# Kernel tuning notes

Measured on AMD Instinct MI355X. Metric: run time of the kernel, lower is better.

The kernel has to match this reference:

```python
import jax, jax.numpy as jnp
import numpy as np

B, S, H = 4, 16, 4096          # batch, new query tokens, hidden
NH, NKV, HD = 32, 8, 128       # query heads, kv heads, head_dim
PAST = 8192                    # cached kv length
ROPE_BASE = 10000.0


def setup_inputs() -> dict:
    key = jax.random.key(0)
    ks = jax.random.split(key, 7)
    wscale = 0.02
    hidden_states = jax.random.normal(ks[0], (B, S, H), jnp.float32)
    k_cache = jax.random.normal(ks[1], (B, PAST, NKV, HD), jnp.float32)
    v_cache = jax.random.normal(ks[2], (B, PAST, NKV, HD), jnp.float32)
    Wq = jax.random.normal(ks[3], (H, NH * HD), jnp.float32) * wscale
    Wk = jax.random.normal(ks[4], (H, NKV * HD), jnp.float32) * wscale
    Wv = jax.random.normal(ks[5], (H, NKV * HD), jnp.float32) * wscale
    Wo = jax.random.normal(ks[6], (NH * HD, H), jnp.float32) * wscale
    position_ids = PAST + jnp.tile(jnp.arange(S, dtype=jnp.int32)[None, :], (B, 1))
    return {"hidden_states": hidden_states, "k_cache": k_cache, "v_cache": v_cache,
            "Wq": Wq, "Wk": Wk, "Wv": Wv, "Wo": Wo, "position_ids": position_ids}


def _rotate_half(x):
    h = x.shape[-1] // 2
    return jnp.concatenate([-x[..., h:], x[..., :h]], axis=-1)


def reference(hidden_states, k_cache, v_cache, Wq, Wk, Wv, Wo, position_ids):
    b, s, _ = hidden_states.shape
    # projections -> [b, heads, s, hd]
    q = (hidden_states @ Wq).reshape(b, s, NH, HD).transpose(0, 2, 1, 3)
    k = (hidden_states @ Wk).reshape(b, s, NKV, HD).transpose(0, 2, 1, 3)
    v = (hidden_states @ Wv).reshape(b, s, NKV, HD).transpose(0, 2, 1, 3)
    # RoPE (LlamaRotaryEmbedding: base=10000, half-split rotate)
    inv_freq = 1.0 / (ROPE_BASE ** (jnp.arange(0, HD, 2, dtype=jnp.float32) / HD))
    ang = position_ids.astype(jnp.float32)[..., None] * inv_freq      # [b, s, hd/2]
    emb = jnp.concatenate([ang, ang], axis=-1)                        # [b, s, hd]
    cos = jnp.cos(emb)[:, None]                                       # [b, 1, s, hd]
    sin = jnp.sin(emb)[:, None]
    q = q * cos + _rotate_half(q) * sin
    k = k * cos + _rotate_half(k) * sin
    # kv-cache concat: cache stored [b, past, nkv, hd] -> [b, nkv, K, hd]
    k_all = jnp.concatenate([k_cache.transpose(0, 2, 1, 3), k], axis=2)
    v_all = jnp.concatenate([v_cache.transpose(0, 2, 1, 3), v], axis=2)
    # GQA repeat_kv (repeat_interleave along head dim)
    n_rep = NH // NKV
    k_all = jnp.repeat(k_all, n_rep, axis=1)                          # [b, NH, K, hd]
    v_all = jnp.repeat(v_all, n_rep, axis=1)
    K = k_all.shape[2]
    scale = HD ** -0.5
    scores = jnp.einsum('bhqd,bhkd->bhqk', q, k_all) * scale          # [b, NH, s, K]
    # flash varlen causal with seqlen_q < seqlen_k: bottom-right aligned mask
    allow = jnp.arange(K)[None, :] <= (K - s + jnp.arange(s))[:, None]
    scores = jnp.where(allow, scores, jnp.float32(-1e30))
    probs = jax.nn.softmax(scores, axis=-1)
    attn = jnp.einsum('bhqk,bhkd->bhqd', probs, v_all)                # [b, NH, s, hd]
    attn = attn.transpose(0, 2, 1, 3).reshape(b, s, NH * HD)
    return attn @ Wo
```

## Files before the change

kernel.cpp:

```cpp
#include <hip/hip_runtime.h>

#define BB 4
#define SS 16
#define NH 32
#define NKV 8
#define HD 128
#define PAST 8192
#define KVLEN 8208
#define KSPLIT 8
#define ASPLIT 16
#define CHUNK 513
#define NTILE 9

typedef __attribute__((ext_vector_type(8))) short short8;
typedef __attribute__((ext_vector_type(4))) float f32x4;

__device__ __forceinline__ unsigned short f2bf(float f) {
  unsigned u = __float_as_uint(f);
  u = (u + 0x7FFFu + ((u >> 16) & 1u)) >> 16;
  return (unsigned short)u;
}
__device__ __forceinline__ float bf2f(unsigned short h) {
  return __uint_as_float(((unsigned)h) << 16);
}
__device__ __forceinline__ unsigned cvtpk(float lo, float hi) {
  unsigned r;
  asm("v_cvt_pk_bf16_f32 %0, %1, %2" : "=v"(r) : "v"(lo), "v"(hi));
  return r;
}
__device__ __forceinline__ void st8(void* p, unsigned lo, unsigned hi) {
  *(unsigned long long*)p = (unsigned long long)lo | ((unsigned long long)hi << 32);
}
__device__ __forceinline__ float getc(const float4& v, int c) {
  return c == 0 ? v.x : c == 1 ? v.y : c == 2 ? v.z : v.w;
}
__device__ __forceinline__ int imin(int a, int b) { return a < b ? a : b; }
__device__ __forceinline__ int imax(int a, int b) { return a > b ? a : b; }

__device__ __forceinline__ void bar_lds() {
  asm volatile("s_waitcnt lgkmcnt(0)" ::: "memory");
  __builtin_amdgcn_s_barrier();
  asm volatile("" ::: "memory");
}
__device__ __forceinline__ void wait_lds() {
  asm volatile("s_waitcnt lgkmcnt(0)" ::: "memory");
}

__global__ __launch_bounds__(256) void xconv(const float* __restrict__ X,
                                             unsigned short* __restrict__ XB) {
  int gid = blockIdx.x * 256 + threadIdx.x;
  float4 v = *(const float4*)&X[(size_t)gid * 4];
  ushort4 pk;
  pk.x = f2bf(v.x); pk.y = f2bf(v.y); pk.z = f2bf(v.z); pk.w = f2bf(v.w);
  *(ushort4*)&XB[(size_t)gid * 4] = pk;
}

__global__ __launch_bounds__(256) void gemm_skinny(
    const unsigned short* __restrict__ A,
    const float* __restrict__ W0, const float* __restrict__ W1, const float* __restrict__ W2,
    int nw0, int nw1, int nw2,
    float* __restrict__ part, int Ntot, int kchunk) {
  __shared__ unsigned short Wt[64 * 64];
  const int nt = blockIdx.x, ks = blockIdx.y;
  const int tid = threadIdx.x, lane = tid & 63, w = tid >> 6;
  const int lr = lane & 15, lc = lane >> 4;
  const int n0 = nt * 64;
  const float* W; int wld, wcol;
  if (n0 < nw0) { W = W0; wld = nw0; wcol = n0; }
  else if (n0 < nw0 + nw1) { W = W1; wld = nw1; wcol = n0 - nw0; }
  else { W = W2; wld = nw2; wcol = n0 - nw0 - nw1; }

  f32x4 acc[4];
  #pragma unroll
  for (int mi = 0; mi < 4; ++mi)
    #pragma unroll
    for (int i = 0; i < 4; ++i) acc[mi][i] = 0.f;

  const int qn = tid & 15, qk = tid >> 4;
  const int kb0 = ks * kchunk;
  const int nkt = kchunk / 64;

  float4 wr0, wr1, wr2, wr3;
  {
    const float* wp = &W[(size_t)(kb0 + qk * 4) * wld + wcol + qn * 4];
    wr0 = *(const float4*)(wp);
    wr1 = *(const float4*)(wp + wld);
    wr2 = *(const float4*)(wp + 2 * (size_t)wld);
    wr3 = *(const float4*)(wp + 3 * (size_t)wld);
  }

  for (int kt = 0; kt < nkt; ++kt) {
    const int kb = kb0 + kt * 64;
    #pragma unroll
    for (int c = 0; c < 4; ++c) {
      const int n = qn * 4 + c;
      ushort4 pk;
      pk.x = f2bf(getc(wr0, c)); pk.y = f2bf(getc(wr1, c));
      pk.z = f2bf(getc(wr2, c)); pk.w = f2bf(getc(wr3, c));
      const int byt = n * 128 + ((qk * 8) ^ ((n & 7) << 4));
      *(ushort4*)((char*)Wt + byt) = pk;
    }
    bar_lds();
    if (kt + 1 < nkt) {
      const float* wp = &W[(size_t)(kb + 64 + qk * 4) * wld + wcol + qn * 4];
      wr0 = *(const float4*)(wp);
      wr1 = *(const float4*)(wp + wld);
      wr2 = *(const float4*)(wp + 2 * (size_t)wld);
      wr3 = *(const float4*)(wp + 3 * (size_t)wld);
    }
    #pragma unroll
    for (int kh = 0; kh < 2; ++kh) {
      const int ncol = w * 16 + lr;
      short8 bf = *(const short8*)((char*)Wt + ncol * 128 + ((kh * 64 + lc * 16) ^ ((ncol & 7) << 4)));
      const int kkg = kb + kh * 32 + lc * 8;
      #pragma unroll
      for (int mi = 0; mi < 4; ++mi) {
        short8 af = *(const short8*)&A[(size_t)(mi * 16 + lr) * 4096 + kkg];
        acc[mi] = __builtin_amdgcn_mfma_f32_16x16x32_bf16(af, bf, acc[mi], 0, 0, 0);
      }
    }
    bar_lds();
  }
  #pragma unroll
  for (int mi = 0; mi < 4; ++mi)
    #pragma unroll
    for (int i = 0; i < 4; ++i) {
      const int row = mi * 16 + lc * 4 + i;
      part[((size_t)ks * 64 + row) * Ntot + n0 + w * 16 + lr] = acc[mi][i];
    }
}

__global__ __launch_bounds__(256) void proj_reduce(
    const float* __restrict__ part, const int* __restrict__ posids,
    unsigned short* __restrict__ QR, float* __restrict__ KF,
    float* __restrict__ VF) {
  const int gid = blockIdx.x * 256 + threadIdx.x;
  const int j = gid & 63;
  const int hh = (gid >> 6) % 48;
  const int row = gid / 3072;
  const int b = row >> 4, s = row & 15;
  int col0; bool rope;
  if (hh < 32)      { col0 = hh * 128 + j; rope = true; }
  else if (hh < 40) { col0 = 4096 + (hh - 32) * 128 + j; rope = true; }
  else              { col0 = 5120 + (hh - 40) * 128 + j; rope = false; }
  float v0 = 0.f, v1 = 0.f;
  #pragma unroll
  for (int ks = 0; ks < KSPLIT; ++ks) {
    v0 += part[((size_t)ks * 64 + row) * 6144 + col0];
    v1 += part[((size_t)ks * 64 + row) * 6144 + col0 + 64];
  }
  float o0 = v0, o1 = v1;
  if (rope) {
    const int pos = posids[row];
    const double inv = exp2(-(double)j * (13.287712379549449 / 64.0));
    double th = (double)pos * inv;
    const double TWO_PI = 6.283185307179586476925286766559;
    th -= floor(th / TWO_PI) * TWO_PI;
    float sv, cv;
    sincosf((float)th, &sv, &cv);
    o0 = v0 * cv - v1 * sv;
    o1 = v1 * cv + v0 * sv;
  }
  if (hh < 32) {
    const size_t didx = (((size_t)(b * 32 + hh) * 16 + s) * 128) + j;
    QR[didx] = f2bf(o0);
    QR[didx + 64] = f2bf(o1);
  } else if (hh < 40) {
    const size_t didx = (((size_t)(b * 8 + (hh - 32)) * 16 + s) * 128) + j;
    KF[didx] = o0;
    KF[didx + 64] = o1;
  } else {
    const size_t didx = (((size_t)(b * 8 + (hh - 40)) * 16 + s) * 128) + j;
    VF[didx] = o0;
    VF[didx + 64] = o1;
  }
}

__global__ __launch_bounds__(512, 2) void attn_kernel(
    const float* __restrict__ kc, const float* __restrict__ vc,
    const unsigned short* __restrict__ QR, const float* __restrict__ KF,
    const float* __restrict__ VF,
    float* __restrict__ Opart, float* __restrict__ ML) {
  __shared__ unsigned short Klds[2][64 * 136];
  __shared__ unsigned short Vt[2][128 * 64];
  __shared__ unsigned short Plds[4][16 * 72];

  const int split = blockIdx.x, kvh = blockIdx.y, b = blockIdx.z;
  const int tid = threadIdx.x;
  const int kstart = split * CHUNK;

  if (tid >= 256) {
    const int ptid = tid - 256;
    const int dl = (ptid & 31) * 4;
    const int rk = ptid >> 5;
    const float* kc_base = kc + (((size_t)b * PAST) * NKV + kvh) * HD + dl;
    const float* vc_base = vc + (((size_t)b * PAST) * NKV + kvh) * HD + dl;
    const float* kf_base = KF + (((size_t)b * NKV + kvh) * SS) * HD + dl;
    const float* vf_base = VF + (((size_t)b * NKV + kvh) * SS) * HD + dl;

    auto stage = [&](int kk0, int buf) {
      float4 kpre[8];
      float4 vpre[8];
      #pragma unroll
      for (int pass = 0; pass < 8; ++pass) {
        const int kk = kk0 + pass * 8 + rk;
        const int ts = imin(imax(kk - PAST, 0), SS - 1);
        const float* p = (kk < PAST) ? (kc_base + (size_t)kk * (NKV * HD))
                                     : (kf_base + (size_t)ts * HD);
        kpre[pass] = *(const float4*)p;
      }
      #pragma unroll
      for (int j = 0; j < 8; ++j) {
        const int kk = kk0 + rk * 8 + j;
        const int ts = imin(imax(kk - PAST, 0), SS - 1);
        const float* p = (kk < PAST) ? (vc_base + (size_t)kk * (NKV * HD))
                                     : (vf_base + (size_t)ts * HD);
        vpre[j] = *(const float4*)p;
      }
      #pragma unroll
      for (int pass = 0; pass < 8; ++pass) {
        const int kr = pass * 8 + rk;
        st8((char*)&Klds[buf][0] + kr * 272 + dl * 2,
            cvtpk(kpre[pass].x, kpre[pass].y), cvtpk(kpre[pass].z, kpre[pass].w));
      }
      #pragma unroll
      for (int pp = 0; pp < 2; ++pp) {
        const int krb = rk * 8 + pp * 4;
        #pragma unroll
        for (int c = 0; c < 4; ++c) {
          const int d = dl + c;
          const int g = ((d ^ (d >> 3)) & 7) << 4;
          st8((char*)&Vt[buf][0] + d * 128 + ((krb * 2) ^ g),
              cvtpk(getc(vpre[pp * 4 + 0], c), getc(vpre[pp * 4 + 1], c)),
              cvtpk(getc(vpre[pp * 4 + 2], c), getc(vpre[pp * 4 + 3], c)));
        }
      }
    };

    stage(kstart, 0);
    bar_lds();
    for (int t = 0; t < NTILE; ++t) {
      if (t + 1 < NTILE) stage(kstart + (t + 1) * 64, (t + 1) & 1);
      bar_lds();
    }
  } else {
    const int lane = tid & 63, w = tid >> 6;
    const int lr = lane & 15, lc = lane >> 4;

    short8 qf[4];
    {
      const unsigned short* qb = QR + (((size_t)b * NH + kvh * 4 + w) * SS + lr) * HD;
      #pragma unroll
      for (int kd = 0; kd < 4; ++kd) qf[kd] = *(const short8*)(qb + kd * 32 + lc * 8);
    }

    float m_i[4], l_i[4];
    f32x4 oacc[8];
    #pragma unroll
    for (int i = 0; i < 4; ++i) { m_i[i] = -1e30f; l_i[i] = 0.f; }
    #pragma unroll
    for (int d8 = 0; d8 < 8; ++d8)
      #pragma unroll
      for (int i = 0; i < 4; ++i) oacc[d8][i] = 0.f;

    bar_lds();

    for (int t = 0; t < NTILE; ++t) {
      const int buf = t & 1;
      const int kk0 = kstart + t * 64;
      const int nvalid = imin(64, kstart + CHUNK - kk0);

      f32x4 sacc[4];
      #pragma unroll
      for (int nb = 0; nb < 4; ++nb)
        #pragma unroll
        for (int i = 0; i < 4; ++i) sacc[nb][i] = 0.f;
      #pragma unroll
      for (int kd = 0; kd < 4; ++kd) {
        #pragma unroll
        for (int nb = 0; nb < 4; ++nb) {
          const int key = nb * 16 + lr;
          short8 bf = *(const short8*)((char*)&Klds[buf][0] + key * 272 + kd * 64 + lc * 16);
          sacc[nb] = __builtin_amdgcn_mfma_f32_16x16x32_bf16(qf[kd], bf, sacc[nb], 0, 0, 0);
        }
      }

      const float scl = 0.08838834764831845f;
      float resc[4];
      #pragma unroll
      for (int i = 0; i < 4; ++i) {
        const int s = lc * 4 + i;
        float vv[4];
        #pragma unroll
        for (int nb = 0; nb < 4; ++nb) {
          const int klocal = nb * 16 + lr;
          const int kk = kk0 + klocal;
          const bool ok = (klocal < nvalid) && (kk <= PAST + s);
          vv[nb] = ok ? sacc[nb][i] * scl : -1e30f;
        }
        float mx = fmaxf(fmaxf(vv[0], vv[1]), fmaxf(vv[2], vv[3]));
        mx = fmaxf(mx, __shfl_xor(mx, 1));
        mx = fmaxf(mx, __shfl_xor(mx, 2));
        mx = fmaxf(mx, __shfl_xor(mx, 4));
        mx = fmaxf(mx, __shfl_xor(mx, 8));
        const float mnew = fmaxf(m_i[i], mx);
        const float rs = __expf(m_i[i] - mnew);
        float p0 = __expf(vv[0] - mnew), p1 = __expf(vv[1] - mnew);
        float p2 = __expf(vv[2] - mnew), p3 = __expf(vv[3] - mnew);
        float sum = p0 + p1 + p2 + p3;
        sum += __shfl_xor(sum, 1);
        sum += __shfl_xor(sum, 2);
        sum += __shfl_xor(sum, 4);
        sum += __shfl_xor(sum, 8);
        l_i[i] = l_i[i] * rs + sum;
        m_i[i] = mnew;
        resc[i] = rs;
        unsigned short* prow = &Plds[w][s * 72];
        prow[0 * 16 + lr] = f2bf(p0);
        prow[1 * 16 + lr] = f2bf(p1);
        prow[2 * 16 + lr] = f2bf(p2);
        prow[3 * 16 + lr] = f2bf(p3);
      }
      #pragma unroll
      for (int d8 = 0; d8 < 8; ++d8)
        #pragma unroll
        for (int i = 0; i < 4; ++i) oacc[d8][i] *= resc[i];

      wait_lds();

      #pragma unroll
      for (int ks2 = 0; ks2 < 2; ++ks2) {
        short8 pf = *(const short8*)((char*)&Plds[w][0] + lr * 144 + ks2 * 64 + lc * 16);
        #pragma unroll
        for (int db = 0; db < 8; ++db) {
          const int d = db * 16 + lr;
          const int g = ((d ^ (d >> 3)) & 7) << 4;
          short8 vf = *(const short8*)((char*)&Vt[buf][0] + d * 128 + ((ks2 * 64 + lc * 16) ^ g));
          oacc[db] = __builtin_amdgcn_mfma_f32_16x16x32_bf16(pf, vf, oacc[db], 0, 0, 0);
        }
      }

      bar_lds();
    }

    const size_t pbase = (((size_t)b * NKV + kvh) * ASPLIT + split) * 64;
    #pragma unroll
    for (int db = 0; db < 8; ++db)
      #pragma unroll
      for (int i = 0; i < 4; ++i) {
        const int row = w * 16 + lc * 4 + i;
        Opart[(pbase + row) * HD + db * 16 + lr] = oacc[db][i];
      }
    if (lr == 0) {
      #pragma unroll
      for (int i = 0; i < 4; ++i) {
        const int row = w * 16 + lc * 4 + i;
        ML[(pbase + row) * 2] = m_i[i];
        ML[(pbase + row) * 2 + 1] = l_i[i];
      }
    }
  }
}

__global__ __launch_bounds__(128) void combine(const float* __restrict__ Opart,
                                               const float* __restrict__ ML,
                                               unsigned short* __restrict__ AT) {
  const int rid = blockIdx.x;
  const int d = threadIdx.x;
  const int s = rid & 15, h = (rid >> 4) & 31, b = rid >> 9;
  const int kvh = h >> 2, g = h & 3;
  const int prow = g * 16 + s;
  const size_t base = ((size_t)b * NKV + kvh) * ASPLIT;
  float ms[ASPLIT], ls[ASPLIT];
  float M = -1e30f;
  #pragma unroll
  for (int sp = 0; sp < ASPLIT; ++sp) {
    ms[sp] = ML[((base + sp) * 64 + prow) * 2];
    ls[sp] = ML[((base + sp) * 64 + prow) * 2 + 1];
    M = fmaxf(M, ms[sp]);
  }
  float denom = 0.f, acc = 0.f;
  #pragma unroll
  for (int sp = 0; sp < ASPLIT; ++sp) {
    const float e = __expf(ms[sp] - M);
    denom += ls[sp] * e;
    acc += e * Opart[((base + sp) * 64 + prow) * HD + d];
  }
  AT[((size_t)(b * 16 + s)) * 4096 + h * 128 + d] = f2bf(acc / denom);
}

__global__ __launch_bounds__(256) void wo_reduce(const float* __restrict__ part,
                                                 float* __restrict__ out) {
  const int gid = blockIdx.x * 256 + threadIdx.x;
  float4 s = {0, 0, 0, 0};
  #pragma unroll
  for (int ks = 0; ks < KSPLIT; ++ks) {
    const float4 v = *(const float4*)&part[(size_t)ks * 262144 + (size_t)gid * 4];
    s.x += v.x; s.y += v.y; s.z += v.z; s.w += v.w;
  }
  *(float4*)&out[(size_t)gid * 4] = s;
}

extern "C" void kernel_launch(void* const* d_in, const int* in_sizes, int n_in,
                              void* d_out, int out_size, void* d_ws, size_t ws_size,
                              hipStream_t stream) {
  (void)in_sizes; (void)n_in; (void)out_size; (void)ws_size;
  const float* hs = (const float*)d_in[0];
  const float* kc = (const float*)d_in[1];
  const float* vc = (const float*)d_in[2];
  const float* Wq = (const float*)d_in[3];
  const float* Wk = (const float*)d_in[4];
  const float* Wv = (const float*)d_in[5];
  const float* Wo = (const float*)d_in[6];
  const int* pos = (const int*)d_in[7];
  float* out = (float*)d_out;
  char* ws = (char*)d_ws;

  unsigned short* XB = (unsigned short*)(ws);
  unsigned short* QR = (unsigned short*)(ws + 0x080000);
  float* KF = (float*)(ws + 0x100000);
  float* VF = (float*)(ws + 0x140000);
  unsigned short* AT = (unsigned short*)(ws + 0x180000);
  float* RED = (float*)(ws + 0x200000);
  float* ML  = (float*)(ws + 0x1300000);

  hipLaunchKernelGGL(xconv, dim3(256), dim3(256), 0, stream, hs, XB);
  hipLaunchKernelGGL(gemm_skinny, dim3(96, KSPLIT), dim3(256), 0, stream,
                     XB, Wq, Wk, Wv, 4096, 1024, 1024, RED, 6144, 4096 / KSPLIT);
  hipLaunchKernelGGL(proj_reduce, dim3(768), dim3(256), 0, stream, RED, pos, QR, KF, VF);
  hipLaunchKernelGGL(attn_kernel, dim3(ASPLIT, NKV, BB), dim3(512), 0, stream,
                     kc, vc, QR, KF, VF, RED, ML);
  hipLaunchKernelGGL(combine, dim3(2048), dim3(128), 0, stream, RED, ML, AT);
  hipLaunchKernelGGL(gemm_skinny, dim3(64, KSPLIT), dim3(256), 0, stream,
                     AT, Wo, Wo, Wo, 4096, 0, 0, RED, 4096, 4096 / KSPLIT);
  hipLaunchKernelGGL(wo_reduce, dim3(256), dim3(256), 0, stream, RED, out);
}
```

Baseline: 137.1 us.

## Prefetch K tiles two ahead in producer warps and raise consumer priority

The producer half of the attention block now issues K-cache loads two tiles ahead into alternating register sets, while V loads stay one tile ahead. It still writes bf16 K and transposed V into double-buffered LDS. The aim is to hide more global-memory latency behind the consumer MFMA work. Consumer waves get a higher scheduling priority via s_setprio, and launch bounds ask for 4 blocks per CU instead of 2. That tighter register limit may cause spills, made worse by the extra prefetch registers.

Measured after the change: 185.7 us. 35.5% more time.

```diff
diff --git a/kernel.cpp b/kernel.cpp
--- a/kernel.cpp
+++ b/kernel.cpp
@@ -176,7 +176,7 @@
   }
 }
 
-__global__ __launch_bounds__(512, 2) void attn_kernel(
+__global__ __launch_bounds__(512, 4) void attn_kernel(
     const float* __restrict__ kc, const float* __restrict__ vc,
     const unsigned short* __restrict__ QR, const float* __restrict__ KF,
     const float* __restrict__ VF,
@@ -198,31 +198,37 @@
     const float* kf_base = KF + (((size_t)b * NKV + kvh) * SS) * HD + dl;
     const float* vf_base = VF + (((size_t)b * NKV + kvh) * SS) * HD + dl;
 
-    auto stage = [&](int kk0, int buf) {
-      float4 kpre[8];
-      float4 vpre[8];
+    float4 kpA[8], kpB[8], vp[8];
+
+    auto issue_K = [&](int kk0, float4* dst) {
       #pragma unroll
       for (int pass = 0; pass < 8; ++pass) {
         const int kk = kk0 + pass * 8 + rk;
         const int ts = imin(imax(kk - PAST, 0), SS - 1);
         const float* p = (kk < PAST) ? (kc_base + (size_t)kk * (NKV * HD))
                                      : (kf_base + (size_t)ts * HD);
-        kpre[pass] = *(const float4*)p;
-      }
+        dst[pass] = *(const float4*)p;
+      }
+    };
+    auto issue_V = [&](int kk0) {
       #pragma unroll
       for (int j = 0; j < 8; ++j) {
         const int kk = kk0 + rk * 8 + j;
         const int ts = imin(imax(kk - PAST, 0), SS - 1);
         const float* p = (kk < PAST) ? (vc_base + (size_t)kk * (NKV * HD))
                                      : (vf_base + (size_t)ts * HD);
-        vpre[j] = *(const float4*)p;
-      }
+        vp[j] = *(const float4*)p;
+      }
+    };
+    auto write_K = [&](const float4* src, int buf) {
       #pragma unroll
       for (int pass = 0; pass < 8; ++pass) {
         const int kr = pass * 8 + rk;
         st8((char*)&Klds[buf][0] + kr * 272 + dl * 2,
-            cvtpk(kpre[pass].x, kpre[pass].y), cvtpk(kpre[pass].z, kpre[pass].w));
-      }
+            cvtpk(src[pass].x, src[pass].y), cvtpk(src[pass].z, src[pass].w));
+      }
+    };
+    auto write_V = [&](int buf) {
       #pragma unroll
       for (int pp = 0; pp < 2; ++pp) {
         const int krb = rk * 8 + pp * 4;
@@ -231,19 +237,35 @@
           const int d = dl + c;
           const int g = ((d ^ (d >> 3)) & 7) << 4;
           st8((char*)&Vt[buf][0] + d * 128 + ((krb * 2) ^ g),
-              cvtpk(getc(vpre[pp * 4 + 0], c), getc(vpre[pp * 4 + 1], c)),
-              cvtpk(getc(vpre[pp * 4 + 2], c), getc(vpre[pp * 4 + 3], c)));
+              cvtpk(getc(vp[pp * 4 + 0], c), getc(vp[pp * 4 + 1], c)),
+              cvtpk(getc(vp[pp * 4 + 2], c), getc(vp[pp * 4 + 3], c)));
         }
       }
     };
 
-    stage(kstart, 0);
+    issue_K(kstart, kpA);
+    issue_V(kstart);
+    write_K(kpA, 0);
+    write_V(0);
+    issue_K(kstart + 64, kpB);
     bar_lds();
+
     for (int t = 0; t < NTILE; ++t) {
-      if (t + 1 < NTILE) stage(kstart + (t + 1) * 64, (t + 1) & 1);
+      const bool haveN = (t + 1 < NTILE);
+      if (haveN) issue_V(kstart + (t + 1) * 64);
+      if (t + 2 < NTILE) {
+        if ((t & 1) == 0) issue_K(kstart + (t + 2) * 64, kpA);
+        else              issue_K(kstart + (t + 2) * 64, kpB);
+      }
+      if (haveN) {
+        if ((t & 1) == 0) write_K(kpB, (t + 1) & 1);
+        else              write_K(kpA, (t + 1) & 1);
+        write_V((t + 1) & 1);
+      }
       bar_lds();
     }
   } else {
+    __builtin_amdgcn_s_setprio(1);
     const int lane = tid & 63, w = tid >> 6;
     const int lr = lane & 15, lc = lane >> 4;
 
```
